# Optimization experiments

Hardware: AMD Instinct MI355X
Metric: run time of the kernel (lower is better)

Reference implementation:

```python
import jax, jax.numpy as jnp
import numpy as np

UNITS = 1024
B, T = 32, 2048


def setup_inputs() -> dict:
    key = jax.random.key(0)
    ks = jax.random.split(key, 8)
    s = 1.0 / np.sqrt(UNITS)
    return {
        "x": jax.random.normal(ks[0], (B, T, UNITS), dtype=jnp.float32),
        "hidden": jax.random.normal(ks[1], (B, UNITS), dtype=jnp.float32),
        "W1_w": jax.random.uniform(ks[2], (UNITS, UNITS), jnp.float32, -s, s),
        "W1_b": jax.random.uniform(ks[3], (UNITS,), jnp.float32, -s, s),
        "W2_w": jax.random.uniform(ks[4], (UNITS, UNITS), jnp.float32, -s, s),
        "W2_b": jax.random.uniform(ks[5], (UNITS,), jnp.float32, -s, s),
        "V_w": jax.random.uniform(ks[6], (1, UNITS), jnp.float32, -s, s),
        "V_b": jax.random.uniform(ks[7], (1,), jnp.float32, -s, s),
    }


def reference(x, hidden, W1_w, W1_b, W2_w, W2_b, V_w, V_b):
    # hidden.squeeze().unsqueeze(1): [B, U] -> [B, 1, U]
    h = hidden[:, None, :]
    # tanh(W1(x) + W2(hidden)): [B, T, U]
    att = jnp.tanh(
        jnp.einsum("btu,vu->btv", x, W1_w) + W1_b
        + jnp.einsum("bsu,vu->bsv", h, W2_w) + W2_b
    )
    # score = V(att): [B, T, 1]
    score = jnp.einsum("btu,ou->bto", att, V_w) + V_b
    # softmax over T, then squeeze().unsqueeze(1): [B, T, 1] -> [B, 1, T]
    attention_weights = jnp.swapaxes(jax.nn.softmax(score, axis=1), 1, 2)
    # bmm([B,1,T], [B,T,U]) -> [B,1,U]; squeeze().unsqueeze(0) -> [1, B, U]
    context_vector = jnp.matmul(attention_weights, x)[:, 0, :][None, :, :]
    return context_vector, attention_weights
```

## Files before the change

kernel.cpp:

```cpp
#include <hip/hip_runtime.h>
#include <hip/hip_bf16.h>
#include <cstdint>
#include <cstddef>

#define UNITS 1024
#define BDIM 32
#define TDIM 2048
#define M_TOT (BDIM*TDIM)
#define KDIM UNITS
#define NDIM UNITS

typedef __attribute__((ext_vector_type(8))) short bf16x8;
typedef __attribute__((ext_vector_type(4))) float f32x4;

__device__ __forceinline__ unsigned short f2bf(float f) {
  unsigned u = __float_as_uint(f);
  u += 0x7fffu + ((u >> 16) & 1u);
  return (unsigned short)(u >> 16);
}
__device__ __forceinline__ float bf2f(unsigned short h) {
  return __uint_as_float(((unsigned)h) << 16);
}

__global__ __launch_bounds__(256) void cvt_kernel(const float* __restrict__ src,
                                                  ushort* __restrict__ dst, int n8) {
  int i = blockIdx.x * blockDim.x + threadIdx.x;
  int stride = gridDim.x * blockDim.x;
  const float4* s4 = (const float4*)src;
  ushort4* d4 = (ushort4*)dst;
  for (; i < n8; i += stride) {
    float4 a = s4[2*i], b = s4[2*i+1];
    ushort4 o0, o1;
    o0.x = f2bf(a.x); o0.y = f2bf(a.y); o0.z = f2bf(a.z); o0.w = f2bf(a.w);
    o1.x = f2bf(b.x); o1.y = f2bf(b.y); o1.z = f2bf(b.z); o1.w = f2bf(b.w);
    d4[2*i] = o0; d4[2*i+1] = o1;
  }
}

__global__ __launch_bounds__(64) void prep_c_kernel(const float* __restrict__ W2w,
                                                    const float* __restrict__ hidden,
                                                    const float* __restrict__ W1b,
                                                    const float* __restrict__ W2b,
                                                    float* __restrict__ c) {
  int v = blockIdx.x;
  int l = threadIdx.x;
  float acc[BDIM];
  #pragma unroll
  for (int b = 0; b < BDIM; b++) acc[b] = 0.f;
  for (int u0 = 0; u0 < UNITS; u0 += 64) {
    float w = W2w[v*UNITS + u0 + l];
    #pragma unroll
    for (int b = 0; b < BDIM; b++) acc[b] += w * hidden[b*UNITS + u0 + l];
  }
  float bias = W1b[v] + W2b[v];
  #pragma unroll
  for (int b = 0; b < BDIM; b++) {
    float s = acc[b];
    #pragma unroll
    for (int off = 32; off > 0; off >>= 1) s += __shfl_xor(s, off);
    if (l == 0) c[b*UNITS + v] = s + bias;
  }
}

__global__ __launch_bounds__(256) void gemm_score_kernel(
    const ushort* __restrict__ A,
    const ushort* __restrict__ W,
    const float* __restrict__ c,
    const float* __restrict__ Vw,
    float* __restrict__ score)
{
  __shared__ ushort As[128*32];
  __shared__ ushort Bs[128*32];
  const int n0 = blockIdx.x * 128;
  const int m0 = blockIdx.y * 128;
  const int bb = m0 >> 11;
  const int tid = threadIdx.x;
  const int wave = tid >> 6;
  const int l = tid & 63;
  const int lrow = l & 15;
  const int lq = l >> 4;
  const int wm = (wave >> 1) * 64;
  const int wn = (wave & 1) * 64;

  f32x4 acc[4][4];
  #pragma unroll
  for (int i = 0; i < 4; i++)
    #pragma unroll
    for (int j = 0; j < 4; j++) acc[i][j] = (f32x4)0.f;

  const int srow = tid >> 2;
  const int skc  = (tid & 3) * 8;
  const ushort* ag0 = A + (size_t)(m0 + srow) * KDIM + skc;
  const ushort* ag1 = A + (size_t)(m0 + 64 + srow) * KDIM + skc;
  const ushort* bg0 = W + (size_t)(n0 + srow) * KDIM + skc;
  const ushort* bg1 = W + (size_t)(n0 + 64 + srow) * KDIM + skc;
  ushort* lA0 = As + wave * 512;
  ushort* lA1 = As + 2048 + wave * 512;
  ushort* lB0 = Bs + wave * 512;
  ushort* lB1 = Bs + 2048 + wave * 512;

  const int aoff = (wm + lrow) * 32 + lq * 8;
  const int boff = (wn + lrow) * 32 + lq * 8;

  for (int k0 = 0; k0 < KDIM; k0 += 32) {
    __builtin_amdgcn_global_load_lds((const __attribute__((address_space(1))) void*)ag0,
                                     (__attribute__((address_space(3))) void*)lA0, 16, 0, 0);
    __builtin_amdgcn_global_load_lds((const __attribute__((address_space(1))) void*)ag1,
                                     (__attribute__((address_space(3))) void*)lA1, 16, 0, 0);
    __builtin_amdgcn_global_load_lds((const __attribute__((address_space(1))) void*)bg0,
                                     (__attribute__((address_space(3))) void*)lB0, 16, 0, 0);
    __builtin_amdgcn_global_load_lds((const __attribute__((address_space(1))) void*)bg1,
                                     (__attribute__((address_space(3))) void*)lB1, 16, 0, 0);
    ag0 += 32; ag1 += 32; bg0 += 32; bg1 += 32;
    __syncthreads();
    bf16x8 af[4], bfv[4];
    #pragma unroll
    for (int i = 0; i < 4; i++) af[i] = *(const bf16x8*)(As + aoff + i * 512);
    #pragma unroll
    for (int j = 0; j < 4; j++) bfv[j] = *(const bf16x8*)(Bs + boff + j * 512);
    #pragma unroll
    for (int i = 0; i < 4; i++)
      #pragma unroll
      for (int j = 0; j < 4; j++)
        acc[i][j] = __builtin_amdgcn_mfma_f32_16x16x32_bf16(af[i], bfv[j], acc[i][j], 0, 0, 0);
    __syncthreads();
  }

  float vw[4], cv[4];
  #pragma unroll
  for (int j = 0; j < 4; j++) {
    int n = n0 + wn + j*16 + lrow;
    vw[j] = Vw[n];
    cv[j] = c[bb*UNITS + n];
  }
  const int mbase = m0 + wm + lq * 4;
  #pragma unroll
  for (int i = 0; i < 4; i++) {
    #pragma unroll
    for (int r = 0; r < 4; r++) {
      float s = 0.f;
      #pragma unroll
      for (int j = 0; j < 4; j++) {
        float xx = acc[i][j][r] + cv[j];
        xx = fminf(fmaxf(xx, -15.f), 15.f);
        float e = __expf(2.f * xx);
        s += vw[j] * __fdividef(e - 1.f, e + 1.f);
      }
      s += __shfl_xor(s, 1);
      s += __shfl_xor(s, 2);
      s += __shfl_xor(s, 4);
      s += __shfl_xor(s, 8);
      if (lrow == 0) atomicAdd(&score[mbase + i*16 + r], s);
    }
  }
}

__global__ __launch_bounds__(256) void softmax_kernel(float* __restrict__ sc,
                                                      float* __restrict__ wout) {
  const int b = blockIdx.x;
  const int tid = threadIdx.x;
  float4* s4 = (float4*)(sc + (size_t)b * TDIM);
  float4 v0 = s4[2*tid], v1 = s4[2*tid+1];
  float mx = fmaxf(fmaxf(fmaxf(v0.x,v0.y),fmaxf(v0.z,v0.w)),
                   fmaxf(fmaxf(v1.x,v1.y),fmaxf(v1.z,v1.w)));
  #pragma unroll
  for (int off = 32; off > 0; off >>= 1) mx = fmaxf(mx, __shfl_xor(mx, off));
  __shared__ float redm[4];
  __shared__ float reds[4];
  if ((tid & 63) == 0) redm[tid >> 6] = mx;
  __syncthreads();
  mx = fmaxf(fmaxf(redm[0], redm[1]), fmaxf(redm[2], redm[3]));
  v0.x = __expf(v0.x - mx); v0.y = __expf(v0.y - mx);
  v0.z = __expf(v0.z - mx); v0.w = __expf(v0.w - mx);
  v1.x = __expf(v1.x - mx); v1.y = __expf(v1.y - mx);
  v1.z = __expf(v1.z - mx); v1.w = __expf(v1.w - mx);
  float sum = v0.x+v0.y+v0.z+v0.w+v1.x+v1.y+v1.z+v1.w;
  #pragma unroll
  for (int off = 32; off > 0; off >>= 1) sum += __shfl_xor(sum, off);
  if ((tid & 63) == 0) reds[tid >> 6] = sum;
  __syncthreads();
  sum = reds[0]+reds[1]+reds[2]+reds[3];
  float inv = 1.f / sum;
  v0.x *= inv; v0.y *= inv; v0.z *= inv; v0.w *= inv;
  v1.x *= inv; v1.y *= inv; v1.z *= inv; v1.w *= inv;
  s4[2*tid] = v0; s4[2*tid+1] = v1;
  float4* w4 = (float4*)(wout + (size_t)b * TDIM);
  w4[2*tid] = v0; w4[2*tid+1] = v1;
}

__global__ __launch_bounds__(256) void context_kernel(const ushort* __restrict__ xb,
                                                      const float* __restrict__ wgt,
                                                      float* __restrict__ ctx) {
  const int tc = blockIdx.x;
  const int b = blockIdx.y;
  const int tid = threadIdx.x;
  const int t0 = tc * 128;
  __shared__ float wl[128];
  if (tid < 128) wl[tid] = wgt[(size_t)b * TDIM + t0 + tid];
  __syncthreads();
  const int u4 = tid * 4;
  float ax = 0.f, ay = 0.f, az = 0.f, aw = 0.f;
  const ushort* xp = xb + ((size_t)b * TDIM + t0) * UNITS + u4;
  for (int i = 0; i < 128; i++) {
    float w = wl[i];
    ushort4 xv = *(const ushort4*)xp;
    ax += w * bf2f(xv.x); ay += w * bf2f(xv.y);
    az += w * bf2f(xv.z); aw += w * bf2f(xv.w);
    xp += UNITS;
  }
  float* o = ctx + (size_t)b * UNITS + u4;
  atomicAdd(o+0, ax); atomicAdd(o+1, ay); atomicAdd(o+2, az); atomicAdd(o+3, aw);
}

extern "C" void kernel_launch(void* const* d_in, const int* in_sizes, int n_in,
                              void* d_out, int out_size, void* d_ws, size_t ws_size,
                              hipStream_t stream) {
  const float* x   = (const float*)d_in[0];
  const float* hid = (const float*)d_in[1];
  const float* W1w = (const float*)d_in[2];
  const float* W1b = (const float*)d_in[3];
  const float* W2w = (const float*)d_in[4];
  const float* W2b = (const float*)d_in[5];
  const float* Vw  = (const float*)d_in[6];
  float* out = (float*)d_out;

  char* ws = (char*)d_ws;
  ushort* xb   = (ushort*)ws;
  ushort* w1b  = (ushort*)(ws + (size_t)M_TOT*KDIM*2);
  float*  cbuf = (float*)(ws + (size_t)M_TOT*KDIM*2 + (size_t)NDIM*KDIM*2);
  float*  score= (float*)((char*)cbuf + (size_t)BDIM*NDIM*4);

  hipMemsetAsync(score, 0, (size_t)M_TOT*sizeof(float), stream);
  hipMemsetAsync(d_out, 0, (size_t)BDIM*UNITS*sizeof(float), stream);

  cvt_kernel<<<4096, 256, 0, stream>>>(x, xb, M_TOT*KDIM/8);
  cvt_kernel<<<512, 256, 0, stream>>>(W1w, w1b, NDIM*KDIM/8);
  prep_c_kernel<<<NDIM, 64, 0, stream>>>(W2w, hid, W1b, W2b, cbuf);
  gemm_score_kernel<<<dim3(NDIM/128, M_TOT/128), 256, 0, stream>>>(xb, w1b, cbuf, Vw, score);
  softmax_kernel<<<BDIM, 256, 0, stream>>>(score, out + (size_t)BDIM*UNITS);
  context_kernel<<<dim3(16, BDIM), 256, 0, stream>>>(xb, score, out);
}
```

Measured before the change: 640.2 us.

## Loop each GEMM block over all N columns, drop atomics, and restructure context kernel

Each GEMM block now owns a 128-row M tile and loops over all 1024 output columns in 256-wide passes. It accumulates the V-projected tanh score in registers, so score atomics and the score memset go away. Tanh is rewritten as 1 - 2/(exp2(2x*log2e)+1), using hardware exp2 and rcp with the constant folded into the bias. The LDS layout gets a rotated swizzle to cut bank conflicts, and launch bounds request 2 blocks per CU. The context kernel now has each block own a 128-unit slice over all T, with 16-byte loads and an in-block reduction, which removes the output atomics and memset. The trade-offs are fewer GEMM blocks, more accumulator registers, and removal of the tanh clamp.

```diff
diff --git a/kernel.cpp b/kernel.cpp
--- a/kernel.cpp
+++ b/kernel.cpp
@@ -10,7 +10,10 @@
 #define KDIM UNITS
 #define NDIM UNITS
 
+#define K2LOG2E 2.885390081777927f
+
 typedef __attribute__((ext_vector_type(8))) short bf16x8;
+typedef __attribute__((ext_vector_type(8))) unsigned short ushort8;
 typedef __attribute__((ext_vector_type(4))) float f32x4;
 
 __device__ __forceinline__ unsigned short f2bf(float f) {
@@ -62,7 +65,7 @@
   }
 }
 
-__global__ __launch_bounds__(256) void gemm_score_kernel(
+__global__ __launch_bounds__(256, 2) void gemm_score_kernel(
     const ushort* __restrict__ A,
     const ushort* __restrict__ W,
     const float* __restrict__ c,
@@ -70,9 +73,10 @@
     float* __restrict__ score)
 {
   __shared__ ushort As[128*32];
-  __shared__ ushort Bs[128*32];
-  const int n0 = blockIdx.x * 128;
-  const int m0 = blockIdx.y * 128;
+  __shared__ ushort Bs[256*32];
+  __shared__ float sred[256];
+
+  const int m0 = blockIdx.x * 128;
   const int bb = m0 >> 11;
   const int tid = threadIdx.x;
   const int wave = tid >> 6;
@@ -80,78 +84,111 @@
   const int lrow = l & 15;
   const int lq = l >> 4;
   const int wm = (wave >> 1) * 64;
-  const int wn = (wave & 1) * 64;
-
-  f32x4 acc[4][4];
-  #pragma unroll
-  for (int i = 0; i < 4; i++)
-    #pragma unroll
-    for (int j = 0; j < 4; j++) acc[i][j] = (f32x4)0.f;
+  const int wn = (wave & 1) * 128;
 
   const int srow = tid >> 2;
-  const int skc  = (tid & 3) * 8;
-  const ushort* ag0 = A + (size_t)(m0 + srow) * KDIM + skc;
-  const ushort* ag1 = A + (size_t)(m0 + 64 + srow) * KDIM + skc;
-  const ushort* bg0 = W + (size_t)(n0 + srow) * KDIM + skc;
-  const ushort* bg1 = W + (size_t)(n0 + 64 + srow) * KDIM + skc;
+  const int scol = ((tid & 3) - (tid >> 3)) & 3;
+  const int skc  = scol * 8;
+  const int slot = (lq + (lrow >> 1)) & 3;
+  const int aoff = (wm + lrow) * 32 + slot * 8;
+  const int boff = (wn + lrow) * 32 + slot * 8;
+
   ushort* lA0 = As + wave * 512;
   ushort* lA1 = As + 2048 + wave * 512;
   ushort* lB0 = Bs + wave * 512;
   ushort* lB1 = Bs + 2048 + wave * 512;
-
-  const int aoff = (wm + lrow) * 32 + lq * 8;
-  const int boff = (wn + lrow) * 32 + lq * 8;
-
-  for (int k0 = 0; k0 < KDIM; k0 += 32) {
-    __builtin_amdgcn_global_load_lds((const __attribute__((address_space(1))) void*)ag0,
-                                     (__attribute__((address_space(3))) void*)lA0, 16, 0, 0);
-    __builtin_amdgcn_global_load_lds((const __attribute__((address_space(1))) void*)ag1,
-                                     (__attribute__((address_space(3))) void*)lA1, 16, 0, 0);
-    __builtin_amdgcn_global_load_lds((const __attribute__((address_space(1))) void*)bg0,
-                                     (__attribute__((address_space(3))) void*)lB0, 16, 0, 0);
-    __builtin_amdgcn_global_load_lds((const __attribute__((address_space(1))) void*)bg1,
-                                     (__attribute__((address_space(3))) void*)lB1, 16, 0, 0);
-    ag0 += 32; ag1 += 32; bg0 += 32; bg1 += 32;
-    __syncthreads();
-    bf16x8 af[4], bfv[4];
-    #pragma unroll
-    for (int i = 0; i < 4; i++) af[i] = *(const bf16x8*)(As + aoff + i * 512);
-    #pragma unroll
-    for (int j = 0; j < 4; j++) bfv[j] = *(const bf16x8*)(Bs + boff + j * 512);
+  ushort* lB2 = Bs + 4096 + wave * 512;
+  ushort* lB3 = Bs + 6144 + wave * 512;
+
+  float sacc[4][4];
+  #pragma unroll
+  for (int i = 0; i < 4; i++)
+    #pragma unroll
+    for (int r = 0; r < 4; r++) sacc[i][r] = 0.f;
+  float vws = 0.f;
+
+  for (int np = 0; np < 4; np++) {
+    const int n0p = np * 256;
+    const ushort* ag0 = A + (size_t)(m0 + srow) * KDIM + skc;
+    const ushort* ag1 = ag0 + (size_t)64 * KDIM;
+    const ushort* wg0 = W + (size_t)(n0p + srow) * KDIM + skc;
+    const ushort* wg1 = wg0 + (size_t)64 * KDIM;
+    const ushort* wg2 = wg0 + (size_t)128 * KDIM;
+    const ushort* wg3 = wg0 + (size_t)192 * KDIM;
+
+    f32x4 acc[4][8];
     #pragma unroll
     for (int i = 0; i < 4; i++)
       #pragma unroll
-      for (int j = 0; j < 4; j++)
-        acc[i][j] = __builtin_amdgcn_mfma_f32_16x16x32_bf16(af[i], bfv[j], acc[i][j], 0, 0, 0);
-    __syncthreads();
-  }
-
-  float vw[4], cv[4];
-  #pragma unroll
-  for (int j = 0; j < 4; j++) {
-    int n = n0 + wn + j*16 + lrow;
-    vw[j] = Vw[n];
-    cv[j] = c[bb*UNITS + n];
-  }
-  const int mbase = m0 + wm + lq * 4;
-  #pragma unroll
-  for (int i = 0; i < 4; i++) {
+      for (int j = 0; j < 8; j++) acc[i][j] = (f32x4)0.f;
+
+    for (int k0 = 0; k0 < KDIM; k0 += 32) {
+      __builtin_amdgcn_global_load_lds((const __attribute__((address_space(1))) void*)ag0,
+                                       (__attribute__((address_space(3))) void*)lA0, 16, 0, 0);
+      __builtin_amdgcn_global_load_lds((const __attribute__((address_space(1))) void*)ag1,
+                                       (__attribute__((address_space(3))) void*)lA1, 16, 0, 0);
+      __builtin_amdgcn_global_load_lds((const __attribute__((address_space(1))) void*)wg0,
+                                       (__attribute__((address_space(3))) void*)lB0, 16, 0, 0);
+      __builtin_amdgcn_global_load_lds((const __attribute__((address_space(1))) void*)wg1,
+                                       (__attribute__((address_space(3))) void*)lB1, 16, 0, 0);
+      __builtin_amdgcn_global_load_lds((const __attribute__((address_space(1))) void*)wg2,
+                                       (__attribute__((address_space(3))) void*)lB2, 16, 0, 0);
+      __builtin_amdgcn_global_load_lds((const __attribute__((address_space(1))) void*)wg3,
+                                       (__attribute__((address_space(3))) void*)lB3, 16, 0, 0);
+      ag0 += 32; ag1 += 32; wg0 += 32; wg1 += 32; wg2 += 32; wg3 += 32;
+      __syncthreads();
+      bf16x8 af[4], bfv[8];
+      #pragma unroll
+      for (int i = 0; i < 4; i++) af[i] = *(const bf16x8*)(As + aoff + i * 512);
+      #pragma unroll
+      for (int j = 0; j < 8; j++) bfv[j] = *(const bf16x8*)(Bs + boff + j * 512);
+      #pragma unroll
+      for (int i = 0; i < 4; i++)
+        #pragma unroll
+        for (int j = 0; j < 8; j++)
+          acc[i][j] = __builtin_amdgcn_mfma_f32_16x16x32_bf16(af[i], bfv[j], acc[i][j], 0, 0, 0);
+      __syncthreads();
+    }
+
+    float vw8[8], ck8[8];
+    #pragma unroll
+    for (int j = 0; j < 8; j++) {
+      int n = n0p + wn + j * 16 + lrow;
+      float v = Vw[n];
+      vw8[j] = v;
+      vws += v;
+      ck8[j] = c[bb * NDIM + n] * K2LOG2E;
+    }
+    #pragma unroll
+    for (int i = 0; i < 4; i++)
+      #pragma unroll
+      for (int j = 0; j < 8; j++)
+        #pragma unroll
+        for (int r = 0; r < 4; r++) {
+          float t = __builtin_fmaf(acc[i][j][r], K2LOG2E, ck8[j]);
+          float e = __builtin_amdgcn_exp2f(t);
+          float rr = __builtin_amdgcn_rcpf(e + 1.f);
+          sacc[i][r] = __builtin_fmaf(vw8[j], rr, sacc[i][r]);
+        }
+  }
+
+  #pragma unroll
+  for (int i = 0; i < 4; i++)
     #pragma unroll
     for (int r = 0; r < 4; r++) {
-      float s = 0.f;
-      #pragma unroll
-      for (int j = 0; j < 4; j++) {
-        float xx = acc[i][j][r] + cv[j];
-        xx = fminf(fmaxf(xx, -15.f), 15.f);
-        float e = __expf(2.f * xx);
-        s += vw[j] * __fdividef(e - 1.f, e + 1.f);
-      }
+      float s = vws - 2.f * sacc[i][r];
       s += __shfl_xor(s, 1);
       s += __shfl_xor(s, 2);
       s += __shfl_xor(s, 4);
       s += __shfl_xor(s, 8);
-      if (lrow == 0) atomicAdd(&score[mbase + i*16 + r], s);
+      if (lrow == 0) sred[wave * 64 + i * 16 + lq * 4 + r] = s;
     }
+  __syncthreads();
+  if (tid < 128) {
+    int half = tid >> 6;
+    int ml = tid & 63;
+    float v = sred[half * 128 + ml] + sred[half * 128 + 64 + ml];
+    score[m0 + tid] = v;
   }
 }
 
@@ -191,25 +228,54 @@
 __global__ __launch_bounds__(256) void context_kernel(const ushort* __restrict__ xb,
                                                       const float* __restrict__ wgt,
                                                       float* __restrict__ ctx) {
-  const int tc = blockIdx.x;
+  const int uc = blockIdx.x;
   const int b = blockIdx.y;
   const int tid = threadIdx.x;
-  const int t0 = tc * 128;
-  __shared__ float wl[128];
-  if (tid < 128) wl[tid] = wgt[(size_t)b * TDIM + t0 + tid];
-  __syncthreads();
-  const int u4 = tid * 4;
-  float ax = 0.f, ay = 0.f, az = 0.f, aw = 0.f;
-  const ushort* xp = xb + ((size_t)b * TDIM + t0) * UNITS + u4;
-  for (int i = 0; i < 128; i++) {
-    float w = wl[i];
-    ushort4 xv = *(const ushort4*)xp;
-    ax += w * bf2f(xv.x); ay += w * bf2f(xv.y);
-    az += w * bf2f(xv.z); aw += w * bf2f(xv.w);
-    xp += UNITS;
-  }
-  float* o = ctx + (size_t)b * UNITS + u4;
-  atomicAdd(o+0, ax); atomicAdd(o+1, ay); atomicAdd(o+2, az); atomicAdd(o+3, aw);
+  __shared__ float wl[TDIM];
+  {
+    const float4* wsrc = (const float4*)(wgt + (size_t)b * TDIM);
+    float4* wdst = (float4*)wl;
+    wdst[tid] = wsrc[tid];
+    wdst[tid + 256] = wsrc[tid + 256];
+  }
+  __syncthreads();
+  const int ut = tid & 15;
+  const int tr = tid >> 4;
+  const ushort* xp = xb + (size_t)b * TDIM * UNITS + uc * 128 + ut * 8;
+  float a8[8];
+  #pragma unroll
+  for (int e = 0; e < 8; e++) a8[e] = 0.f;
+  for (int t = tr; t < TDIM; t += 64) {
+    ushort8 x0 = *(const ushort8*)(xp + (size_t)(t     ) * UNITS);
+    ushort8 x1 = *(const ushort8*)(xp + (size_t)(t + 16) * UNITS);
+    ushort8 x2 = *(const ushort8*)(xp + (size_t)(t + 32) * UNITS);
+    ushort8 x3 = *(const ushort8*)(xp + (size_t)(t + 48) * UNITS);
+    float w0 = wl[t], w1 = wl[t+16], w2 = wl[t+32], w3 = wl[t+48];
+    #pragma unroll
+    for (int e = 0; e < 8; e++) {
+      a8[e] += w0 * bf2f(x0[e]);
+      a8[e] += w1 * bf2f(x1[e]);
+      a8[e] += w2 * bf2f(x2[e]);
+      a8[e] += w3 * bf2f(x3[e]);
+    }
+  }
+  #pragma unroll
+  for (int e = 0; e < 8; e++) {
+    a8[e] += __shfl_xor(a8[e], 16);
+    a8[e] += __shfl_xor(a8[e], 32);
+  }
+  __shared__ float red[512];
+  const int wave = tid >> 6;
+  const int l = tid & 63;
+  if (l < 16) {
+    #pragma unroll
+    for (int e = 0; e < 8; e++) red[wave * 128 + l * 8 + e] = a8[e];
+  }
+  __syncthreads();
+  if (tid < 128) {
+    float v = red[tid] + red[128 + tid] + red[256 + tid] + red[384 + tid];
+    ctx[(size_t)b * UNITS + uc * 128 + tid] = v;
+  }
 }
 
 extern "C" void kernel_launch(void* const* d_in, const int* in_sizes, int n_in,
@@ -230,13 +296,10 @@
   float*  cbuf = (float*)(ws + (size_t)M_TOT*KDIM*2 + (size_t)NDIM*KDIM*2);
   float*  score= (float*)((char*)cbuf + (size_t)BDIM*NDIM*4);
 
-  hipMemsetAsync(score, 0, (size_t)M_TOT*sizeof(float), stream);
-  hipMemsetAsync(d_out, 0, (size_t)BDIM*UNITS*sizeof(float), stream);
-
   cvt_kernel<<<4096, 256, 0, stream>>>(x, xb, M_TOT*KDIM/8);
   cvt_kernel<<<512, 256, 0, stream>>>(W1w, w1b, NDIM*KDIM/8);
   prep_c_kernel<<<NDIM, 64, 0, stream>>>(W2w, hid, W1b, W2b, cbuf);
-  gemm_score_kernel<<<dim3(NDIM/128, M_TOT/128), 256, 0, stream>>>(xb, w1b, cbuf, Vw, score);
+  gemm_score_kernel<<<M_TOT/128, 256, 0, stream>>>(xb, w1b, cbuf, Vw, score);
   softmax_kernel<<<BDIM, 256, 0, stream>>>(score, out + (size_t)BDIM*UNITS);
-  context_kernel<<<dim3(16, BDIM), 256, 0, stream>>>(xb, score, out);
-}
+  context_kernel<<<dim3(8, BDIM), 256, 0, stream>>>(xb, score, out);
+}
```

After: 580.9 us. 9.3% less time.
